# Kernel optimization log

Measured on AMD Instinct MI355X. Metric: run time of the kernel, lower is better.

## Reference

```python
import jax, jax.numpy as jnp
import numpy as np

SIM_THRESHOLD = 0.6  # recall() only returns a memory if best cosine sim > 0.6
EPS = 1e-8           # torch cosine_similarity eps


def setup_inputs() -> dict:
    key = jax.random.key(0)
    k1, k2, k3, k4 = jax.random.split(key, 4)
    B, N, D = 256, 50000, 1024
    query = jax.random.normal(k1, (B, D), dtype=jnp.float32)
    memories = jax.random.normal(k2, (N, D), dtype=jnp.float32)
    # decoder = nn.Linear(D, D): y = x @ W^T + b
    scale = 1.0 / np.sqrt(D)
    dec_w = jax.random.uniform(k3, (D, D), dtype=jnp.float32, minval=-scale, maxval=scale)
    dec_b = jax.random.uniform(k4, (D,), dtype=jnp.float32, minval=-scale, maxval=scale)
    return {"query": query, "memories": memories, "dec_w": dec_w, "dec_b": dec_b}


def reference(query, memories, dec_w, dec_b):
    # Batched version of recall(): cosine sim of each query vs all stored
    # memory embeddings, argmax, threshold at 0.6, decode winner.
    # query: [B, D], memories: [N, D]
    qnorm = jnp.linalg.norm(query, axis=-1)      # [B]
    mnorm = jnp.linalg.norm(memories, axis=-1)   # [N]
    dots = jnp.einsum('bd,nd->bn', query, memories)  # [B, N]
    sims = dots / jnp.maximum(qnorm[:, None] * mnorm[None, :], EPS)
    best_idx = jnp.argmax(sims, axis=-1)                              # [B]
    best_sim = jnp.take_along_axis(sims, best_idx[:, None], axis=1)[:, 0]  # [B]
    best_emb = memories[best_idx]                                     # [B, D]
    decoded = best_emb @ dec_w.T + dec_b                              # [B, D]
    # Original returns None below threshold; represent as zeros row.
    out = jnp.where(best_sim[:, None] > SIM_THRESHOLD, decoded, jnp.zeros_like(decoded))
    return out
```

## Files before the change

kernel.cpp:

```cpp
#include <hip/hip_runtime.h>
#include <stdint.h>

#define N_MEM   50000
#define DDIM    1024
#define MQ      256
#define BK      64
#define NT      64
#define NCHUNK  ((N_MEM + NT - 1) / NT)
#define KCHUNKS (DDIM / BK)
#define THREADS 256
#define SIM_TH  0.6f
#define NEGINF  (-3.0e38f)

typedef __attribute__((ext_vector_type(8))) short short8;
typedef __attribute__((ext_vector_type(4))) float f32x4;

__device__ __forceinline__ unsigned short f2bf(float x) {
  union { float f; unsigned int u; } a; a.f = x;
  unsigned int r = (a.u + 0x7fffu + ((a.u >> 16) & 1u)) >> 16;
  return (unsigned short)r;
}

__device__ __forceinline__ void dma16(const void* g, void* l) {
  __builtin_amdgcn_global_load_lds(
      (const __attribute__((address_space(1))) unsigned int*)g,
      (__attribute__((address_space(3))) unsigned int*)l, 16, 0, 0);
}

__global__ __launch_bounds__(256) void prep_kernel(
    const float* __restrict__ q, unsigned short* __restrict__ qbf,
    float* __restrict__ qnorm) {
  const int m = blockIdx.x;
  const int t = threadIdx.x;
  const f32x4 v = *(const f32x4*)(q + (size_t)m * DDIM + t * 4);
  const int k = t * 4;
  const int kc = k >> 6;
  const int jb = (k >> 3) & 7;
  const int half = (k >> 2) & 1;
  ushort4 h;
  h.x = f2bf(v.x); h.y = f2bf(v.y); h.z = f2bf(v.z); h.w = f2bf(v.w);
  *(ushort4*)(qbf + (size_t)kc * (MQ * BK) + m * 64 + ((jb ^ (m & 7)) * 8) + half * 4) = h;

  float ss = v.x * v.x + v.y * v.y + v.z * v.z + v.w * v.w;
  #pragma unroll
  for (int off = 1; off < 64; off <<= 1) ss += __shfl_xor(ss, off);
  __shared__ float red[4];
  if ((t & 63) == 0) red[t >> 6] = ss;
  __syncthreads();
  if (t == 0) qnorm[m] = sqrtf(red[0] + red[1] + red[2] + red[3]);
}

__global__ __launch_bounds__(THREADS, 3) void sim_argmax_kernel(
    const float* __restrict__ mem, const unsigned short* __restrict__ qbf,
    float* __restrict__ pmax, int* __restrict__ pidx) {
  __shared__ unsigned short As[MQ * BK];
  __shared__ unsigned short Bs[NT * BK];
  __shared__ float rinv[NT];

  const int t = threadIdx.x;
  const int lane = t & 63;
  const int w = t >> 6;
  const int c = blockIdx.x;
  const int n0 = c * NT;

  const int br = t >> 2;
  const int bj = t & 3;

  f32x4 acc[4][4];
  #pragma unroll
  for (int mi = 0; mi < 4; ++mi)
    #pragma unroll
    for (int ni = 0; ni < 4; ++ni)
      acc[mi][ni] = (f32x4){0.f, 0.f, 0.f, 0.f};

  const bool browok = (n0 + br) < N_MEM;
  const float* browp = mem + (size_t)(n0 + br) * DDIM;
  float sumsq = 0.f;

  for (int kc = 0; kc < KCHUNKS; ++kc) {
    const unsigned short* qc = qbf + (size_t)kc * (MQ * BK);
    #pragma unroll
    for (int i = 0; i < 8; ++i)
      dma16(qc + i * 2048 + t * 8, (void*)(As + i * 2048 + t * 8));

    f32x4 v[4];
    const float* p = browp + kc * BK + bj * 4;
    #pragma unroll
    for (int i = 0; i < 4; ++i) {
      if (browok) v[i] = *(const f32x4*)(p + i * 16);
      else        v[i] = (f32x4){0.f, 0.f, 0.f, 0.f};
      sumsq += v[i].x * v[i].x + v[i].y * v[i].y + v[i].z * v[i].z + v[i].w * v[i].w;
      const int col = i * 16 + bj * 4;
      const int jb = col >> 3;
      const int half = (col >> 2) & 1;
      ushort4 h;
      h.x = f2bf(v[i].x); h.y = f2bf(v[i].y); h.z = f2bf(v[i].z); h.w = f2bf(v[i].w);
      *(ushort4*)(Bs + br * 64 + ((jb ^ (br & 7)) * 8) + half * 4) = h;
    }
    __syncthreads();

    {
      const int quad = lane >> 4, li = lane & 15;
      #pragma unroll
      for (int s = 0; s < 2; ++s) {
        const int kb = s * 4 + quad;
        short8 af[4], bfr[4];
        #pragma unroll
        for (int mi = 0; mi < 4; ++mi) {
          const int m = w * 64 + mi * 16 + li;
          af[mi] = *(const short8*)(As + m * 64 + ((kb ^ (m & 7)) * 8));
        }
        #pragma unroll
        for (int ni = 0; ni < 4; ++ni) {
          const int n = ni * 16 + li;
          bfr[ni] = *(const short8*)(Bs + n * 64 + ((kb ^ (n & 7)) * 8));
        }
        #pragma unroll
        for (int mi = 0; mi < 4; ++mi)
          #pragma unroll
          for (int ni = 0; ni < 4; ++ni)
            acc[mi][ni] = __builtin_amdgcn_mfma_f32_16x16x32_bf16(
                af[mi], bfr[ni], acc[mi][ni], 0, 0, 0);
      }
    }
    __syncthreads();
  }

  sumsq += __shfl_xor(sumsq, 1);
  sumsq += __shfl_xor(sumsq, 2);
  if (bj == 0) rinv[br] = browok ? rsqrtf(fmaxf(sumsq, 1e-30f)) : 0.f;
  __syncthreads();

  {
    const int quad = lane >> 4, li = lane & 15;
    float rv[4]; int gn[4];
    #pragma unroll
    for (int ni = 0; ni < 4; ++ni) {
      const int nl = ni * 16 + li;
      rv[ni] = rinv[nl];
      gn[ni] = n0 + nl;
    }
    #pragma unroll
    for (int mi = 0; mi < 4; ++mi) {
      #pragma unroll
      for (int r = 0; r < 4; ++r) {
        float best = NEGINF; int bi = 0x7fffffff;
        #pragma unroll
        for (int ni = 0; ni < 4; ++ni) {
          float vv = acc[mi][ni][r] * rv[ni];
          vv = (gn[ni] < N_MEM) ? vv : NEGINF;
          if (vv > best || (vv == best && gn[ni] < bi)) { best = vv; bi = gn[ni]; }
        }
        #pragma unroll
        for (int off = 1; off < 16; off <<= 1) {
          const float ov = __shfl_xor(best, off);
          const int oi = __shfl_xor(bi, off);
          if (ov > best || (ov == best && oi < bi)) { best = ov; bi = oi; }
        }
        if (li == 0) {
          const int row = w * 64 + mi * 16 + quad * 4 + r;
          pmax[(size_t)c * MQ + row] = best;
          pidx[(size_t)c * MQ + row] = bi;
        }
      }
    }
  }
}

__global__ __launch_bounds__(256) void finalize_kernel(
    const float* __restrict__ mem, const float* __restrict__ dec_w,
    const float* __restrict__ dec_b, const float* __restrict__ qnorm,
    const float* __restrict__ pmax, const int* __restrict__ pidx,
    float* __restrict__ out) {
  const int b = blockIdx.x;
  const int t = threadIdx.x;
  float best = NEGINF; int bi = 0x7fffffff;
  for (int c = t; c < NCHUNK; c += 256) {
    const float v = pmax[(size_t)c * MQ + b];
    const int i = pidx[(size_t)c * MQ + b];
    if (v > best || (v == best && i < bi)) { best = v; bi = i; }
  }
  #pragma unroll
  for (int off = 1; off < 64; off <<= 1) {
    const float ov = __shfl_xor(best, off);
    const int oi = __shfl_xor(bi, off);
    if (ov > best || (ov == best && oi < bi)) { best = ov; bi = oi; }
  }
  __shared__ float sv[4]; __shared__ int si[4];
  __shared__ float sbest; __shared__ int sbi;
  if ((t & 63) == 0) { sv[t >> 6] = best; si[t >> 6] = bi; }
  __syncthreads();
  if (t == 0) {
    float bb = sv[0]; int ii = si[0];
    #pragma unroll
    for (int k = 1; k < 4; ++k)
      if (sv[k] > bb || (sv[k] == bb && si[k] < ii)) { bb = sv[k]; ii = si[k]; }
    sbest = bb; sbi = ii;
  }
  __syncthreads();

  const float sim = sbest / fmaxf(qnorm[b], 1e-20f);
  if (sim > SIM_TH) {
    __shared__ float ms[DDIM];
    *(f32x4*)(ms + t * 4) = *(const f32x4*)(mem + (size_t)sbi * DDIM + t * 4);
    __syncthreads();
    #pragma unroll
    for (int jj = 0; jj < 4; ++jj) {
      const int j = jj * 256 + t;
      const float* wr = dec_w + (size_t)j * DDIM;
      float s = dec_b[j];
      for (int k = 0; k < DDIM; k += 4) {
        const f32x4 a = *(const f32x4*)(ms + k);
        const f32x4 ww = *(const f32x4*)(wr + k);
        s += a.x * ww.x + a.y * ww.y + a.z * ww.z + a.w * ww.w;
      }
      out[(size_t)b * DDIM + j] = s;
    }
  } else {
    *(f32x4*)(out + (size_t)b * DDIM + t * 4) = (f32x4){0.f, 0.f, 0.f, 0.f};
  }
}

extern "C" void kernel_launch(void* const* d_in, const int* in_sizes, int n_in,
                              void* d_out, int out_size, void* d_ws, size_t ws_size,
                              hipStream_t stream) {
  const float* query = (const float*)d_in[0];
  const float* mem   = (const float*)d_in[1];
  const float* dec_w = (const float*)d_in[2];
  const float* dec_b = (const float*)d_in[3];
  float* out = (float*)d_out;

  char* ws = (char*)d_ws;
  unsigned short* qbf = (unsigned short*)ws;
  float* qnorm = (float*)(ws + 524288);
  float* pmax  = (float*)(ws + 525312);
  int*   pidx  = (int*)(ws + 525312 + (size_t)NCHUNK * MQ * 4);

  hipLaunchKernelGGL(prep_kernel, dim3(MQ), dim3(256), 0, stream,
                     query, qbf, qnorm);
  hipLaunchKernelGGL(sim_argmax_kernel, dim3(NCHUNK), dim3(THREADS), 0, stream,
                     mem, qbf, pmax, pidx);
  hipLaunchKernelGGL(finalize_kernel, dim3(MQ), dim3(256), 0, stream,
                     mem, dec_w, dec_b, qnorm, pmax, pidx, out);
}
```

Measured before the change: 345.3 us.

## Switch similarity GEMM to FP8 with double-buffered query tiles and full-row memory staging

```diff
diff --git a/kernel.cpp b/kernel.cpp
--- a/kernel.cpp
+++ b/kernel.cpp
@@ -5,20 +5,48 @@
 #define DDIM    1024
 #define MQ      256
 #define BK      64
-#define NT      64
-#define NCHUNK  ((N_MEM + NT - 1) / NT)
+#define NT      32
+#define NBLK    ((N_MEM + NT - 1) / NT)
 #define KCHUNKS (DDIM / BK)
 #define THREADS 256
 #define SIM_TH  0.6f
 #define NEGINF  (-3.0e38f)
-
-typedef __attribute__((ext_vector_type(8))) short short8;
+#define ACHUNK  (MQ * BK)
+
 typedef __attribute__((ext_vector_type(4))) float f32x4;
 
-__device__ __forceinline__ unsigned short f2bf(float x) {
-  union { float f; unsigned int u; } a; a.f = x;
-  unsigned int r = (a.u + 0x7fffu + ((a.u >> 16) & 1u)) >> 16;
-  return (unsigned short)r;
+#if defined(__has_builtin)
+#if __has_builtin(__builtin_amdgcn_cvt_pk_fp8_f32)
+#define HAVE_CVT_PK_FP8 1
+#endif
+#endif
+
+__device__ __forceinline__ unsigned int f2e4m3_1(float x) {
+  unsigned int u = __float_as_uint(x);
+  unsigned int s = (u >> 24) & 0x80u;
+  unsigned int a = u & 0x7fffffffu;
+  if (a >= 0x43E00000u) return s | 0x7Eu;
+  if (a < 0x3C800000u) {
+    float ax = __uint_as_float(a);
+    unsigned int q = (unsigned int)(ax * 512.0f + 0.5f);
+    return s | q;
+  }
+  a += 0x0007FFFFu + ((a >> 20) & 1u);
+  int E = (int)(a >> 23) - 127 + 7;
+  unsigned int m = (a >> 20) & 7u;
+  if (E > 15 || (E == 15 && m == 7u)) return s | 0x7Eu;
+  return s | ((unsigned int)E << 3) | m;
+}
+
+__device__ __forceinline__ int pack4_fp8(f32x4 v) {
+#ifdef HAVE_CVT_PK_FP8
+  int pk = __builtin_amdgcn_cvt_pk_fp8_f32(v.x, v.y, 0, false);
+  pk = __builtin_amdgcn_cvt_pk_fp8_f32(v.z, v.w, pk, true);
+  return pk;
+#else
+  return (int)(f2e4m3_1(v.x) | (f2e4m3_1(v.y) << 8) |
+               (f2e4m3_1(v.z) << 16) | (f2e4m3_1(v.w) << 24));
+#endif
 }
 
 __device__ __forceinline__ void dma16(const void* g, void* l) {
@@ -28,18 +56,15 @@
 }
 
 __global__ __launch_bounds__(256) void prep_kernel(
-    const float* __restrict__ q, unsigned short* __restrict__ qbf,
+    const float* __restrict__ q, unsigned char* __restrict__ qf8,
     float* __restrict__ qnorm) {
   const int m = blockIdx.x;
   const int t = threadIdx.x;
   const f32x4 v = *(const f32x4*)(q + (size_t)m * DDIM + t * 4);
-  const int k = t * 4;
-  const int kc = k >> 6;
-  const int jb = (k >> 3) & 7;
-  const int half = (k >> 2) & 1;
-  ushort4 h;
-  h.x = f2bf(v.x); h.y = f2bf(v.y); h.z = f2bf(v.z); h.w = f2bf(v.w);
-  *(ushort4*)(qbf + (size_t)kc * (MQ * BK) + m * 64 + ((jb ^ (m & 7)) * 8) + half * 4) = h;
+  const int kc = t >> 4;
+  const int kb = (t >> 1) & 7;
+  const int pk = pack4_fp8(v);
+  *(int*)(qf8 + (size_t)kc * ACHUNK + m * 64 + ((kb ^ (m & 7)) * 8) + (t & 1) * 4) = pk;
 
   float ss = v.x * v.x + v.y * v.y + v.z * v.z + v.w * v.w;
   #pragma unroll
@@ -50,92 +75,93 @@
   if (t == 0) qnorm[m] = sqrtf(red[0] + red[1] + red[2] + red[3]);
 }
 
-__global__ __launch_bounds__(THREADS, 3) void sim_argmax_kernel(
-    const float* __restrict__ mem, const unsigned short* __restrict__ qbf,
+__global__ __launch_bounds__(THREADS, 2) void sim_kernel(
+    const float* __restrict__ mem, const unsigned char* __restrict__ qf8,
     float* __restrict__ pmax, int* __restrict__ pidx) {
-  __shared__ unsigned short As[MQ * BK];
-  __shared__ unsigned short Bs[NT * BK];
+  __shared__ unsigned char As[2][ACHUNK];
+  __shared__ unsigned char Bs[NT * DDIM];
   __shared__ float rinv[NT];
 
   const int t = threadIdx.x;
   const int lane = t & 63;
   const int w = t >> 6;
+  const int quad = lane >> 4, li = lane & 15;
   const int c = blockIdx.x;
   const int n0 = c * NT;
 
-  const int br = t >> 2;
-  const int bj = t & 3;
-
-  f32x4 acc[4][4];
+  f32x4 acc[4][2];
   #pragma unroll
   for (int mi = 0; mi < 4; ++mi)
     #pragma unroll
-    for (int ni = 0; ni < 4; ++ni)
+    for (int ni = 0; ni < 2; ++ni)
       acc[mi][ni] = (f32x4){0.f, 0.f, 0.f, 0.f};
 
-  const bool browok = (n0 + br) < N_MEM;
-  const float* browp = mem + (size_t)(n0 + br) * DDIM;
-  float sumsq = 0.f;
+  #pragma unroll
+  for (int i = 0; i < 4; ++i)
+    dma16(qf8 + i * 4096 + t * 16, (void*)(&As[0][i * 4096 + t * 16]));
+
+  for (int p = 0; p < 8; ++p) {
+    const int r = w * 8 + p;
+    const int gn = n0 + r;
+    const bool ok = gn < N_MEM;
+    const float* rp = mem + (size_t)gn * DDIM;
+    float ss = 0.f;
+    #pragma unroll
+    for (int sp = 0; sp < 4; ++sp) {
+      f32x4 v;
+      if (ok) v = *(const f32x4*)(rp + sp * 256 + lane * 4);
+      else    v = (f32x4){0.f, 0.f, 0.f, 0.f};
+      ss += v.x * v.x + v.y * v.y + v.z * v.z + v.w * v.w;
+      const int col = sp * 256 + lane * 4;
+      const int kb = col >> 3;
+      const int kb2 = (kb & ~7) | ((kb ^ r) & 7);
+      *(int*)(Bs + r * DDIM + kb2 * 8 + (col & 7)) = pack4_fp8(v);
+    }
+    #pragma unroll
+    for (int off = 1; off < 64; off <<= 1) ss += __shfl_xor(ss, off);
+    if (lane == 0) rinv[r] = ok ? rsqrtf(fmaxf(ss, 1e-30f)) : 0.f;
+  }
+  __syncthreads();
 
   for (int kc = 0; kc < KCHUNKS; ++kc) {
-    const unsigned short* qc = qbf + (size_t)kc * (MQ * BK);
-    #pragma unroll
-    for (int i = 0; i < 8; ++i)
-      dma16(qc + i * 2048 + t * 8, (void*)(As + i * 2048 + t * 8));
-
-    f32x4 v[4];
-    const float* p = browp + kc * BK + bj * 4;
-    #pragma unroll
-    for (int i = 0; i < 4; ++i) {
-      if (browok) v[i] = *(const f32x4*)(p + i * 16);
-      else        v[i] = (f32x4){0.f, 0.f, 0.f, 0.f};
-      sumsq += v[i].x * v[i].x + v[i].y * v[i].y + v[i].z * v[i].z + v[i].w * v[i].w;
-      const int col = i * 16 + bj * 4;
-      const int jb = col >> 3;
-      const int half = (col >> 2) & 1;
-      ushort4 h;
-      h.x = f2bf(v[i].x); h.y = f2bf(v[i].y); h.z = f2bf(v[i].z); h.w = f2bf(v[i].w);
-      *(ushort4*)(Bs + br * 64 + ((jb ^ (br & 7)) * 8) + half * 4) = h;
+    const unsigned char* a_cur = As[kc & 1];
+    if (kc + 1 < KCHUNKS) {
+      const unsigned char* qc = qf8 + (size_t)(kc + 1) * ACHUNK;
+      unsigned char* dst = As[(kc + 1) & 1];
+      #pragma unroll
+      for (int i = 0; i < 4; ++i)
+        dma16(qc + i * 4096 + t * 16, (void*)(dst + i * 4096 + t * 16));
+    }
+    #pragma unroll
+    for (int s = 0; s < 2; ++s) {
+      const int kb = s * 4 + quad;
+      const int kbg = kc * 8 + kb;
+      long af[4], bf[2];
+      #pragma unroll
+      for (int mi = 0; mi < 4; ++mi) {
+        const int m = w * 64 + mi * 16 + li;
+        af[mi] = *(const long*)(a_cur + m * 64 + ((kb ^ (m & 7)) * 8));
+      }
+      #pragma unroll
+      for (int ni = 0; ni < 2; ++ni) {
+        const int n = ni * 16 + li;
+        const int kb2 = (kbg & ~7) | ((kbg ^ (n & 7)) & 7);
+        bf[ni] = *(const long*)(Bs + n * DDIM + kb2 * 8);
+      }
+      #pragma unroll
+      for (int mi = 0; mi < 4; ++mi)
+        #pragma unroll
+        for (int ni = 0; ni < 2; ++ni)
+          acc[mi][ni] = __builtin_amdgcn_mfma_f32_16x16x32_fp8_fp8(
+              af[mi], bf[ni], acc[mi][ni], 0, 0, 0);
     }
     __syncthreads();
-
-    {
-      const int quad = lane >> 4, li = lane & 15;
-      #pragma unroll
-      for (int s = 0; s < 2; ++s) {
-        const int kb = s * 4 + quad;
-        short8 af[4], bfr[4];
-        #pragma unroll
-        for (int mi = 0; mi < 4; ++mi) {
-          const int m = w * 64 + mi * 16 + li;
-          af[mi] = *(const short8*)(As + m * 64 + ((kb ^ (m & 7)) * 8));
-        }
-        #pragma unroll
-        for (int ni = 0; ni < 4; ++ni) {
-          const int n = ni * 16 + li;
-          bfr[ni] = *(const short8*)(Bs + n * 64 + ((kb ^ (n & 7)) * 8));
-        }
-        #pragma unroll
-        for (int mi = 0; mi < 4; ++mi)
-          #pragma unroll
-          for (int ni = 0; ni < 4; ++ni)
-            acc[mi][ni] = __builtin_amdgcn_mfma_f32_16x16x32_bf16(
-                af[mi], bfr[ni], acc[mi][ni], 0, 0, 0);
-      }
-    }
-    __syncthreads();
-  }
-
-  sumsq += __shfl_xor(sumsq, 1);
-  sumsq += __shfl_xor(sumsq, 2);
-  if (bj == 0) rinv[br] = browok ? rsqrtf(fmaxf(sumsq, 1e-30f)) : 0.f;
-  __syncthreads();
+  }
 
   {
-    const int quad = lane >> 4, li = lane & 15;
-    float rv[4]; int gn[4];
-    #pragma unroll
-    for (int ni = 0; ni < 4; ++ni) {
+    float rv[2]; int gn[2];
+    #pragma unroll
+    for (int ni = 0; ni < 2; ++ni) {
       const int nl = ni * 16 + li;
       rv[ni] = rinv[nl];
       gn[ni] = n0 + nl;
@@ -146,7 +172,7 @@
       for (int r = 0; r < 4; ++r) {
         float best = NEGINF; int bi = 0x7fffffff;
         #pragma unroll
-        for (int ni = 0; ni < 4; ++ni) {
+        for (int ni = 0; ni < 2; ++ni) {
           float vv = acc[mi][ni][r] * rv[ni];
           vv = (gn[ni] < N_MEM) ? vv : NEGINF;
           if (vv > best || (vv == best && gn[ni] < bi)) { best = vv; bi = gn[ni]; }
@@ -159,8 +185,8 @@
         }
         if (li == 0) {
           const int row = w * 64 + mi * 16 + quad * 4 + r;
-          pmax[(size_t)c * MQ + row] = best;
-          pidx[(size_t)c * MQ + row] = bi;
+          pmax[(size_t)row * NBLK + c] = best;
+          pidx[(size_t)row * NBLK + c] = bi;
         }
       }
     }
@@ -175,9 +201,9 @@
   const int b = blockIdx.x;
   const int t = threadIdx.x;
   float best = NEGINF; int bi = 0x7fffffff;
-  for (int c = t; c < NCHUNK; c += 256) {
-    const float v = pmax[(size_t)c * MQ + b];
-    const int i = pidx[(size_t)c * MQ + b];
+  for (int c = t; c < NBLK; c += 256) {
+    const float v = pmax[(size_t)b * NBLK + c];
+    const int i = pidx[(size_t)b * NBLK + c];
     if (v > best || (v == best && i < bi)) { best = v; bi = i; }
   }
   #pragma unroll
@@ -231,15 +257,15 @@
   float* out = (float*)d_out;
 
   char* ws = (char*)d_ws;
-  unsigned short* qbf = (unsigned short*)ws;
-  float* qnorm = (float*)(ws + 524288);
-  float* pmax  = (float*)(ws + 525312);
-  int*   pidx  = (int*)(ws + 525312 + (size_t)NCHUNK * MQ * 4);
+  unsigned char* qf8 = (unsigned char*)ws;
+  float* qnorm = (float*)(ws + 262144);
+  float* pmax  = (float*)(ws + 263168);
+  int*   pidx  = (int*)(ws + 263168 + (size_t)MQ * NBLK * 4);
 
   hipLaunchKernelGGL(prep_kernel, dim3(MQ), dim3(256), 0, stream,
-                     query, qbf, qnorm);
-  hipLaunchKernelGGL(sim_argmax_kernel, dim3(NCHUNK), dim3(THREADS), 0, stream,
-                     mem, qbf, pmax, pidx);
+                     query, qf8, qnorm);
+  hipLaunchKernelGGL(sim_kernel, dim3(NBLK), dim3(THREADS), 0, stream,
+                     mem, qf8, pmax, pidx);
   hipLaunchKernelGGL(finalize_kernel, dim3(MQ), dim3(256), 0, stream,
                      mem, dec_w, dec_b, qnorm, pmax, pidx, out);
 }
```

Result: slower. 375.1 us (+8.6%).
